# Kernel optimization log

Hardware: AMD Instinct MI355X
Metric: run time of the kernel (lower is better)

Reference implementation:

```python
import jax, jax.numpy as jnp
import numpy as np

N, D, E, NNZ = 200000, 128, 1024, 1600000


def setup_inputs() -> dict:
    key = jax.random.key(0)
    ks = jax.random.split(key, 8)
    x = jax.random.normal(ks[0], (N, D), jnp.float32)
    tb_W = jax.random.normal(ks[1], (5, 3, D, D), jnp.float32) * 0.05
    tb_b = jax.random.normal(ks[2], (5, 3, D), jnp.float32) * 0.05
    hg_W = jax.random.normal(ks[3], (2, D, D), jnp.float32) * 0.05
    hg_b = jax.random.normal(ks[4], (2, D), jnp.float32) * 0.05
    hyperedge_attr = jax.random.normal(ks[5], (E, D), jnp.float32)
    node_idx = jax.random.randint(ks[6], (NNZ,), 0, N)
    edge_idx = jax.random.randint(ks[7], (NNZ,), 0, E)
    return dict(x=x, tb_W=tb_W, tb_b=tb_b, hg_W=hg_W, hg_b=hg_b,
                hyperedge_attr=hyperedge_attr, node_idx=node_idx,
                edge_idx=edge_idx, num_hyperedges=E)


def _time_block(x, W, b):
    # 1x1 Conv2d over channel dim == per-node linear. W:[3,D,D], b:[3,D]
    c1 = x @ W[0] + b[0]
    c2 = x @ W[1] + b[1]
    c3 = x @ W[2] + b[2]
    return jax.nn.relu(c1 + jax.nn.sigmoid(c2) + c3)


def _hypergraph_conv(x, node_idx, edge_idx, W, b, num_nodes, num_edges):
    # PyG HypergraphConv, use_attention=False (heads=1):
    # out = D^{-1} H B H^T (x W) + b, H given as COO (node_idx, edge_idx)
    xp = x @ W
    ones = jnp.ones(node_idx.shape[0], xp.dtype)
    Dn = jax.ops.segment_sum(ones, node_idx, num_segments=num_nodes)
    Dn = jnp.where(Dn > 0, 1.0 / Dn, 0.0)
    Be = jax.ops.segment_sum(ones, edge_idx, num_segments=num_edges)
    Be = jnp.where(Be > 0, 1.0 / Be, 0.0)
    # node -> hyperedge aggregation, normalized by 1/B_e
    m = jax.ops.segment_sum(xp[node_idx], edge_idx, num_segments=num_edges) * Be[:, None]
    # hyperedge -> node aggregation, normalized by 1/D_v
    out = jax.ops.segment_sum(m[edge_idx], node_idx, num_segments=num_nodes) * Dn[:, None]
    return out + b


def reference(x, tb_W, tb_b, hg_W, hg_b, hyperedge_attr, node_idx, edge_idx, num_hyperedges):
    # hyperedge_attr is unused when use_attention=False (faithful to PyG)
    n = x.shape[0]
    h = _time_block(x, tb_W[0], tb_b[0])
    h = _hypergraph_conv(h, node_idx, edge_idx, hg_W[0], hg_b[0], n, num_hyperedges)
    h = _time_block(h, tb_W[1], tb_b[1])
    h = _time_block(h, tb_W[2], tb_b[2])
    h = _hypergraph_conv(h, node_idx, edge_idx, hg_W[1], hg_b[1], n, num_hyperedges)
    h = _time_block(h, tb_W[3], tb_b[3])
    h = _time_block(h, tb_W[4], tb_b[4])
    return h
```

## Files before the change

kernel.cpp:

```cpp
#include <hip/hip_runtime.h>
#include <stdint.h>

#define N_NODES 200000
#define DIM     128
#define N_EDGES 1024
#define NNZ_C   1600000
#define NT_TILES 6250

#define NBLK   250
#define CHUNK  6400
#define ITERS  25
#define NCB    196

#define NG_BLOCKS 2048
#define NG_WAVES  (NG_BLOCKS*4)

typedef __attribute__((ext_vector_type(8))) short short8;
typedef __attribute__((ext_vector_type(4))) float f32x4;

__device__ __forceinline__ float u2f(uint32_t u){ union{uint32_t u;float f;} x; x.u=u; return x.f; }
__device__ __forceinline__ uint32_t f2u(float f){ union{uint32_t u;float f;} x; x.f=f; return x.u; }
__device__ __forceinline__ unsigned short f2bf(float f){
  uint32_t u = f2u(f);
  u += 0x7fffu + ((u >> 16) & 1u);
  return (unsigned short)(u >> 16);
}

__global__ void prep_tb_w(const float* __restrict__ W, short* __restrict__ Wt){
  int i = blockIdx.x*256 + threadIdx.x;
  if (i >= 5*384*128) return;
  int k   = i & 127;
  int col = (i >> 7) % 384;
  int s   = i / 49152;
  int j = col >> 7, n = col & 127;
  Wt[i] = (short)f2bf(W[((s*3 + j)*128 + k)*128 + n]);
}
__global__ void prep_hg_wf(const float* __restrict__ W, float* __restrict__ Wtf){
  int i = blockIdx.x*256 + threadIdx.x;
  if (i >= 2*128*128) return;
  int k = i & 127;
  int n = (i >> 7) & 127;
  int g = i >> 14;
  Wtf[i] = W[(g*128 + k)*128 + n];
}

__global__ __launch_bounds__(256) void hist_kernel(
    const int* __restrict__ nidx, const int* __restrict__ eidx,
    int* __restrict__ ebh, int* __restrict__ nbh)
{
  __shared__ int eh[N_EDGES];
  __shared__ int nh[NCB];
  int tid = threadIdx.x, blk = blockIdx.x;
  #pragma unroll
  for (int l = tid; l < N_EDGES; l += 256) eh[l] = 0;
  for (int l = tid; l < NCB; l += 256) nh[l] = 0;
  __syncthreads();
  int base = blk*CHUNK;
  for (int it = 0; it < ITERS; it++){
    int i = base + it*256 + tid;
    atomicAdd(&eh[eidx[i]], 1);
    atomicAdd(&nh[nidx[i] >> 10], 1);
  }
  __syncthreads();
  for (int l = tid; l < N_EDGES; l += 256) ebh[blk*N_EDGES + l] = eh[l];
  for (int l = tid; l < NCB; l += 256) nbh[blk*NCB + l] = nh[l];
}

__global__ __launch_bounds__(1024) void escan_kernel(
    int* __restrict__ ebh, int* __restrict__ eoff)
{
  __shared__ int sc[1024];
  int e = threadIdx.x;
  int total = 0;
  #pragma unroll 10
  for (int b = 0; b < NBLK; b++){
    int idx = b*N_EDGES + e;
    int t = ebh[idx];
    ebh[idx] = total;
    total += t;
  }
  sc[e] = total; __syncthreads();
  for (int off=1; off<1024; off<<=1){
    int v = (e >= off) ? sc[e-off] : 0;
    __syncthreads();
    sc[e] += v;
    __syncthreads();
  }
  int base = sc[e] - total;
  eoff[e] = base;
  if (e == 1023) eoff[1024] = sc[1023];
  #pragma unroll 10
  for (int b = 0; b < NBLK; b++) ebh[b*N_EDGES + e] += base;
}

__global__ __launch_bounds__(256) void nscan_kernel(
    int* __restrict__ nbh, int* __restrict__ cbase)
{
  __shared__ int sc[256];
  int c = threadIdx.x;
  int total = 0;
  if (c < NCB){
    #pragma unroll 10
    for (int b = 0; b < NBLK; b++){
      int idx = b*NCB + c;
      int t = nbh[idx];
      nbh[idx] = total;
      total += t;
    }
  }
  sc[c] = (c < NCB) ? total : 0; __syncthreads();
  for (int off=1; off<256; off<<=1){
    int v = (c >= off) ? sc[c-off] : 0;
    __syncthreads();
    sc[c] += v;
    __syncthreads();
  }
  int base = sc[c] - ((c < NCB) ? total : 0);
  if (c < NCB) cbase[c] = base;
  if (c == NCB-1) cbase[NCB] = sc[c];
  __syncthreads();
  if (c < NCB){
    #pragma unroll 10
    for (int b = 0; b < NBLK; b++) nbh[b*NCB + c] += base;
  }
}

__global__ __launch_bounds__(256) void scatter_kernel(
    const int* __restrict__ nidx, const int* __restrict__ eidx,
    const int* __restrict__ ebh, const int* __restrict__ nbh,
    int* __restrict__ enodes, uint32_t* __restrict__ pairs)
{
  __shared__ int cure[N_EDGES];
  __shared__ int curn[NCB];
  int tid = threadIdx.x, blk = blockIdx.x;
  for (int l = tid; l < N_EDGES; l += 256) cure[l] = ebh[blk*N_EDGES + l];
  for (int l = tid; l < NCB; l += 256)     curn[l] = nbh[blk*NCB + l];
  __syncthreads();
  int base = blk*CHUNK;
  for (int it = 0; it < ITERS; it++){
    int i = base + it*256 + tid;
    int v = nidx[i], e = eidx[i];
    int pe = atomicAdd(&cure[e], 1);
    enodes[pe] = v;
    int pn = atomicAdd(&curn[v >> 10], 1);
    pairs[pn] = ((uint32_t)v << 10) | (uint32_t)e;
  }
}

__global__ __launch_bounds__(256) void node_build_kernel(
    const uint32_t* __restrict__ pairs, const int* __restrict__ cbase,
    int* __restrict__ noff, int* __restrict__ nedges)
{
  __shared__ int cnt[1024];
  __shared__ int off[1024];
  __shared__ int part[256];
  int tid = threadIdx.x, c = blockIdx.x;
  int n0 = c << 10;
  int nloc = min(1024, N_NODES - n0);
  int s = cbase[c], e = cbase[c+1];
  #pragma unroll
  for (int l = tid; l < 1024; l += 256) cnt[l] = 0;
  __syncthreads();
  for (int i = s + tid; i < e; i += 256)
    atomicAdd(&cnt[(pairs[i] >> 10) & 1023], 1);
  __syncthreads();
  int c0 = cnt[tid*4], c1 = cnt[tid*4+1], c2 = cnt[tid*4+2], c3 = cnt[tid*4+3];
  int sum = c0+c1+c2+c3;
  part[tid] = sum; __syncthreads();
  for (int o=1; o<256; o<<=1){
    int v = (tid >= o) ? part[tid-o] : 0;
    __syncthreads();
    part[tid] += v;
    __syncthreads();
  }
  int pb = part[tid] - sum;
  off[tid*4]   = pb;
  off[tid*4+1] = pb + c0;
  off[tid*4+2] = pb + c0 + c1;
  off[tid*4+3] = pb + c0 + c1 + c2;
  __syncthreads();
  for (int l = tid; l < nloc; l += 256) noff[n0 + l] = s + off[l];
  if (c == 0 && tid == 0) noff[N_NODES] = NNZ_C;
  __syncthreads();
  for (int i = s + tid; i < e; i += 256){
    uint32_t p = pairs[i];
    int local = (p >> 10) & 1023;
    int pos = s + atomicAdd(&off[local], 1);
    nedges[pos] = (int)(p & 1023);
  }
}

template<bool IN_F32, int OUT_MODE>
__global__ __launch_bounds__(256, 2) void gemm_kernel(
    const void* __restrict__ in, void* __restrict__ out,
    const short* __restrict__ Wt, const float* __restrict__ bias)
{
  __shared__ short Atile[32][136];
  const int tid  = threadIdx.x;
  const int lane = tid & 63;
  const int w    = tid >> 6;
  const int l15  = lane & 15;
  const int quad = lane >> 4;

  short8 bfrag[3][2][4];
  #pragma unroll
  for (int j = 0; j < 3; j++)
    #pragma unroll
    for (int nt = 0; nt < 2; nt++){
      const short* bp = Wt + (j*128 + w*32 + nt*16 + l15)*128 + quad*8;
      #pragma unroll
      for (int ks = 0; ks < 4; ks++)
        bfrag[j][nt][ks] = *(const short8*)(bp + ks*32);
    }

  float bv[3][2];
  #pragma unroll
  for (int j = 0; j < 3; j++)
    #pragma unroll
    for (int nt = 0; nt < 2; nt++)
      bv[j][nt] = bias[j*128 + w*32 + nt*16 + l15];

  const int arow = tid >> 3;
  const int aseg = (tid & 7) * 2;

  short8 pre0, pre1;
  auto loadA = [&](int t){
    int off = (t*32 + arow)*128 + aseg*8;
    if (IN_F32){
      const float* f = (const float*)in + off;
      f32x4 q0 = ((const f32x4*)f)[0];
      f32x4 q1 = ((const f32x4*)f)[1];
      f32x4 q2 = ((const f32x4*)f)[2];
      f32x4 q3 = ((const f32x4*)f)[3];
      short8 t0, t1;
      #pragma unroll
      for (int u = 0; u < 4; u++){
        t0[u]   = (short)f2bf(q0[u]);
        t0[u+4] = (short)f2bf(q1[u]);
        t1[u]   = (short)f2bf(q2[u]);
        t1[u+4] = (short)f2bf(q3[u]);
      }
      pre0 = t0; pre1 = t1;
    } else {
      const short* hp = (const short*)in + off;
      pre0 = *(const short8*)hp;
      pre1 = *(const short8*)(hp + 8);
    }
  };

  int t = blockIdx.x;
  loadA(t);
  for (;;){
    __syncthreads();
    *(short8*)&Atile[arow][aseg*8]     = pre0;
    *(short8*)&Atile[arow][aseg*8 + 8] = pre1;
    __syncthreads();
    int tn = t + gridDim.x;
    if (tn < NT_TILES) loadA(tn);

    const int base = t*32;
    #pragma unroll
    for (int rt = 0; rt < 2; rt++){
      short8 af[4];
      #pragma unroll
      for (int ks = 0; ks < 4; ks++)
        af[ks] = *(const short8*)&Atile[rt*16 + l15][ks*32 + quad*8];

      f32x4 acc[3][2];
      #pragma unroll
      for (int j = 0; j < 3; j++)
        #pragma unroll
        for (int nt = 0; nt < 2; nt++){
          acc[j][nt] = (f32x4){0.f, 0.f, 0.f, 0.f};
          #pragma unroll
          for (int ks = 0; ks < 4; ks++)
            acc[j][nt] = __builtin_amdgcn_mfma_f32_16x16x32_bf16(
                af[ks], bfrag[j][nt][ks], acc[j][nt], 0, 0, 0);
        }

      #pragma unroll
      for (int nt = 0; nt < 2; nt++){
        int col = w*32 + nt*16 + l15;
        #pragma unroll
        for (int r = 0; r < 4; r++){
          int row = base + rt*16 + quad*4 + r;
          float c2 = acc[1][nt][r] + bv[1][nt];
          float sg = 1.f / (1.f + __expf(-c2));
          float v = acc[0][nt][r] + bv[0][nt] + sg + acc[2][nt][r] + bv[2][nt];
          v = fmaxf(v, 0.f);
          if (OUT_MODE == 1) ((float*)out)[row*128 + col] = v;
          else if (OUT_MODE == 0) ((unsigned short*)out)[row*128 + col] = f2bf(v);
          else {
            int pk = __builtin_amdgcn_cvt_pk_fp8_f32(v, v, 0, false);
            ((unsigned char*)out)[row*128 + col] = (unsigned char)(pk & 0xff);
          }
        }
      }
    }
    if (tn >= NT_TILES) break;
    t = tn;
  }
}

__global__ __launch_bounds__(256) void edge_gather_kernel(
    const unsigned char* __restrict__ h8, const int* __restrict__ eoff,
    const int* __restrict__ enodes, float* __restrict__ s_e)
{
  int bid = blockIdx.x;
  int e = bid >> 2, q = bid & 3;
  int s = eoff[e], en = eoff[e+1];
  int tid = threadIdx.x;
  int rr   = tid >> 5;
  int slot = q*8 + rr;
  int ch   = tid & 31;
  float a0=0.f, a1=0.f, a2=0.f, a3=0.f;
  int i = s + slot;
  int nd = (i < en) ? enodes[i] : 0;
  while (i < en){
    int inx = i + 32;
    int ndn = (inx < en) ? enodes[inx] : 0;
    uint32_t raw = *(const uint32_t*)(h8 + (size_t)nd*128 + ch*4);
    auto lo = __builtin_amdgcn_cvt_pk_f32_fp8(raw, false);
    auto hi = __builtin_amdgcn_cvt_pk_f32_fp8(raw, true);
    a0 += lo[0]; a1 += lo[1]; a2 += hi[0]; a3 += hi[1];
    i = inx; nd = ndn;
  }
  __shared__ float red[8][132];
  red[rr][ch*4+0]=a0; red[rr][ch*4+1]=a1; red[rr][ch*4+2]=a2; red[rr][ch*4+3]=a3;
  __syncthreads();
  if (tid < 128){
    float sum = 0.f;
    #pragma unroll
    for (int r = 0; r < 8; r++) sum += red[r][tid];
    atomicAdd(&s_e[e*128 + tid], sum);
  }
}

__global__ __launch_bounds__(128) void egemm_kernel(
    const float* __restrict__ s_e, const int* __restrict__ eoff,
    const float* __restrict__ Wtf, uint32_t* __restrict__ mbf)
{
  __shared__ float srow[128];
  __shared__ float sacc[128];
  int e = blockIdx.x, n = threadIdx.x;
  srow[n] = s_e[e*128 + n];
  __syncthreads();
  int deg = eoff[e+1] - eoff[e];
  float be = deg > 0 ? 1.f/(float)deg : 0.f;
  const f32x4* w4 = (const f32x4*)(Wtf + n*128);
  float acc = 0.f;
  #pragma unroll
  for (int k = 0; k < 32; k++){
    f32x4 qv = w4[k];
    acc += qv[0]*srow[k*4] + qv[1]*srow[k*4+1] + qv[2]*srow[k*4+2] + qv[3]*srow[k*4+3];
  }
  sacc[n] = acc * be;
  __syncthreads();
  if (n < 64){
    uint32_t lo = f2bf(sacc[2*n]);
    uint32_t hi = f2bf(sacc[2*n+1]);
    mbf[e*64 + n] = (hi << 16) | lo;
  }
}

__global__ __launch_bounds__(256) void node_gather_kernel(
    const uint32_t* __restrict__ mbf, const int* __restrict__ noff,
    const int* __restrict__ nedges, const float* __restrict__ hb,
    uint32_t* __restrict__ outp)
{
  int wid  = (blockIdx.x << 2) | (threadIdx.x >> 6);
  int lane = threadIdx.x & 63;
  float b0 = hb[2*lane], b1 = hb[2*lane+1];
  const int K = (N_NODES + NG_WAVES - 1) / NG_WAVES;
  int v0 = wid * K;
  int v1 = min(v0 + K, N_NODES);
  for (int v = v0; v < v1; v++){
    int s = noff[v], e = noff[v+1];
    float a0 = 0.f, a1 = 0.f, a2 = 0.f, a3 = 0.f;
    int i = s;
    for (; i + 4 <= e; i += 4){
      int e0 = nedges[i],   e1 = nedges[i+1];
      int e2 = nedges[i+2], e3 = nedges[i+3];
      uint32_t r0 = mbf[(e0 << 6) | lane];
      uint32_t r1 = mbf[(e1 << 6) | lane];
      uint32_t r2 = mbf[(e2 << 6) | lane];
      uint32_t r3 = mbf[(e3 << 6) | lane];
      a0 += u2f(r0 << 16); a1 += u2f(r0 & 0xffff0000u);
      a2 += u2f(r1 << 16); a3 += u2f(r1 & 0xffff0000u);
      a0 += u2f(r2 << 16); a1 += u2f(r2 & 0xffff0000u);
      a2 += u2f(r3 << 16); a3 += u2f(r3 & 0xffff0000u);
    }
    for (; i < e; i++){
      int ed = nedges[i];
      uint32_t r = mbf[(ed << 6) | lane];
      a0 += u2f(r << 16); a1 += u2f(r & 0xffff0000u);
    }
    a0 += a2; a1 += a3;
    float dn = (e > s) ? 1.f/(float)(e - s) : 0.f;
    uint32_t lo = f2bf(a0*dn + b0);
    uint32_t hi = f2bf(a1*dn + b1);
    outp[((size_t)v << 6) | lane] = (hi << 16) | lo;
  }
}

extern "C" void kernel_launch(void* const* d_in, const int* in_sizes, int n_in,
                              void* d_out, int out_size, void* d_ws, size_t ws_size,
                              hipStream_t stream)
{
  (void)in_sizes; (void)n_in; (void)out_size; (void)ws_size;
  const float* x   = (const float*)d_in[0];
  const float* tbW = (const float*)d_in[1];
  const float* tbb = (const float*)d_in[2];
  const float* hgW = (const float*)d_in[3];
  const float* hgb = (const float*)d_in[4];
  const int* nidx  = (const int*)d_in[6];
  const int* eidx  = (const int*)d_in[7];
  float* out = (float*)d_out;

  char* p = (char*)d_ws;
  auto alloc = [&](size_t sz){ void* r = (void*)p; p += (sz + 255) & ~(size_t)255; return r; };
  unsigned short* hA = (unsigned short*)alloc((size_t)N_NODES*DIM*2);
  unsigned short* hB = (unsigned short*)alloc((size_t)N_NODES*DIM*2);
  unsigned char*  h8 = (unsigned char*)alloc((size_t)N_NODES*DIM);
  float* s_e  = (float*)alloc((size_t)N_EDGES*DIM*4);
  uint32_t* mbf = (uint32_t*)alloc((size_t)N_EDGES*64*4);
  short* WtTb = (short*)alloc((size_t)5*384*128*2);
  float* Wtf  = (float*)alloc((size_t)2*128*128*4);
  int* ebh  = (int*)alloc((size_t)NBLK*N_EDGES*4);
  int* nbh  = (int*)alloc((size_t)NBLK*NCB*4);
  int* eoff = (int*)alloc((N_EDGES+1)*4);
  int* cbase= (int*)alloc((NCB+1)*4);
  int* noff = (int*)alloc((size_t)(N_NODES+1)*4);
  int* enodes = (int*)alloc((size_t)NNZ_C*4);
  int* nedges = (int*)alloc((size_t)NNZ_C*4);
  uint32_t* pairs = (uint32_t*)h8;

  prep_tb_w<<<960, 256, 0, stream>>>(tbW, WtTb);
  prep_hg_wf<<<128, 256, 0, stream>>>(hgW, Wtf);

  hist_kernel<<<NBLK, 256, 0, stream>>>(nidx, eidx, ebh, nbh);
  escan_kernel<<<1, 1024, 0, stream>>>(ebh, eoff);
  nscan_kernel<<<1, 256, 0, stream>>>(nbh, cbase);
  scatter_kernel<<<NBLK, 256, 0, stream>>>(nidx, eidx, ebh, nbh, enodes, pairs);
  node_build_kernel<<<NCB, 256, 0, stream>>>(pairs, cbase, noff, nedges);

  gemm_kernel<true, 2><<<1024, 256, 0, stream>>>(x, h8, WtTb, tbb);
  hipMemsetAsync(s_e, 0, (size_t)N_EDGES*DIM*4, stream);
  edge_gather_kernel<<<4*N_EDGES, 256, 0, stream>>>(h8, eoff, enodes, s_e);
  egemm_kernel<<<N_EDGES, 128, 0, stream>>>(s_e, eoff, Wtf, mbf);
  node_gather_kernel<<<NG_BLOCKS, 256, 0, stream>>>(mbf, noff, nedges, hgb, (uint32_t*)hA);
  gemm_kernel<false, 0><<<1024, 256, 0, stream>>>(hA, hB, WtTb + 1*49152, tbb + 1*384);
  gemm_kernel<false, 2><<<1024, 256, 0, stream>>>(hB, h8, WtTb + 2*49152, tbb + 2*384);
  hipMemsetAsync(s_e, 0, (size_t)N_EDGES*DIM*4, stream);
  edge_gather_kernel<<<4*N_EDGES, 256, 0, stream>>>(h8, eoff, enodes, s_e);
  egemm_kernel<<<N_EDGES, 128, 0, stream>>>(s_e, eoff, Wtf + 16384, mbf);
  node_gather_kernel<<<NG_BLOCKS, 256, 0, stream>>>(mbf, noff, nedges, hgb + 128, (uint32_t*)hA);
  gemm_kernel<false, 0><<<1024, 256, 0, stream>>>(hA, hB, WtTb + 3*49152, tbb + 3*384);
  gemm_kernel<false, 1><<<1024, 256, 0, stream>>>(hB, out, WtTb + 4*49152, tbb + 4*384);
}
```

Before: 768.1 us.

## Restructure edge gather: one block per edge, 16-byte loads, no atomics

```diff
diff --git a/kernel.cpp b/kernel.cpp
--- a/kernel.cpp
+++ b/kernel.cpp
@@ -302,37 +302,68 @@
   }
 }
 
+__device__ __forceinline__ void acc16(float* a, uint4 r){
+  uint32_t w[4] = {r.x, r.y, r.z, r.w};
+  #pragma unroll
+  for (int q = 0; q < 4; q++){
+    auto lo = __builtin_amdgcn_cvt_pk_f32_fp8(w[q], false);
+    auto hi = __builtin_amdgcn_cvt_pk_f32_fp8(w[q], true);
+    a[q*4+0] += lo[0]; a[q*4+1] += lo[1]; a[q*4+2] += hi[0]; a[q*4+3] += hi[1];
+  }
+}
+
 __global__ __launch_bounds__(256) void edge_gather_kernel(
     const unsigned char* __restrict__ h8, const int* __restrict__ eoff,
     const int* __restrict__ enodes, float* __restrict__ s_e)
 {
-  int bid = blockIdx.x;
-  int e = bid >> 2, q = bid & 3;
+  int e = blockIdx.x;
   int s = eoff[e], en = eoff[e+1];
-  int tid = threadIdx.x;
-  int rr   = tid >> 5;
-  int slot = q*8 + rr;
-  int ch   = tid & 31;
-  float a0=0.f, a1=0.f, a2=0.f, a3=0.f;
-  int i = s + slot;
-  int nd = (i < en) ? enodes[i] : 0;
-  while (i < en){
-    int inx = i + 32;
-    int ndn = (inx < en) ? enodes[inx] : 0;
-    uint32_t raw = *(const uint32_t*)(h8 + (size_t)nd*128 + ch*4);
-    auto lo = __builtin_amdgcn_cvt_pk_f32_fp8(raw, false);
-    auto hi = __builtin_amdgcn_cvt_pk_f32_fp8(raw, true);
-    a0 += lo[0]; a1 += lo[1]; a2 += hi[0]; a3 += hi[1];
-    i = inx; nd = ndn;
-  }
-  __shared__ float red[8][132];
-  red[rr][ch*4+0]=a0; red[rr][ch*4+1]=a1; red[rr][ch*4+2]=a2; red[rr][ch*4+3]=a3;
+  int tid  = threadIdx.x;
+  int slot = tid >> 3;
+  int ch   = tid & 7;
+  const size_t choff = (size_t)ch * 16;
+
+  float a[16];
+  #pragma unroll
+  for (int j = 0; j < 16; j++) a[j] = 0.f;
+
+  int i0 = s + slot;
+  int n0 = (i0      < en) ? enodes[i0]      : -1;
+  int n1 = (i0 + 32 < en) ? enodes[i0 + 32] : -1;
+  int n2 = (i0 + 64 < en) ? enodes[i0 + 64] : -1;
+  int n3 = (i0 + 96 < en) ? enodes[i0 + 96] : -1;
+
+  while (i0 < en){
+    int i1 = i0 + 128;
+    int m0 = (i1      < en) ? enodes[i1]      : -1;
+    int m1 = (i1 + 32 < en) ? enodes[i1 + 32] : -1;
+    int m2 = (i1 + 64 < en) ? enodes[i1 + 64] : -1;
+    int m3 = (i1 + 96 < en) ? enodes[i1 + 96] : -1;
+
+    uint4 r0 = *(const uint4*)(h8 + (((size_t)max(n0,0)) << 7) + choff);
+    uint4 r1 = *(const uint4*)(h8 + (((size_t)max(n1,0)) << 7) + choff);
+    uint4 r2 = *(const uint4*)(h8 + (((size_t)max(n2,0)) << 7) + choff);
+    uint4 r3 = *(const uint4*)(h8 + (((size_t)max(n3,0)) << 7) + choff);
+    if (n0 < 0) r0 = make_uint4(0,0,0,0);
+    if (n1 < 0) r1 = make_uint4(0,0,0,0);
+    if (n2 < 0) r2 = make_uint4(0,0,0,0);
+    if (n3 < 0) r3 = make_uint4(0,0,0,0);
+
+    acc16(a, r0); acc16(a, r1); acc16(a, r2); acc16(a, r3);
+
+    n0 = m0; n1 = m1; n2 = m2; n3 = m3;
+    i0 = i1;
+  }
+
+  __shared__ float red[32][132];
+  #pragma unroll
+  for (int j = 0; j < 16; j++) red[slot][ch*16 + j] = a[j];
   __syncthreads();
   if (tid < 128){
     float sum = 0.f;
     #pragma unroll
-    for (int r = 0; r < 8; r++) sum += red[r][tid];
-    atomicAdd(&s_e[e*128 + tid], sum);
+    for (int r = 0; r < 32; r++) sum += red[r][tid];
+    s_e[e*128 + tid] = sum;
   }
 }
 
@@ -445,14 +476,12 @@
   node_build_kernel<<<NCB, 256, 0, stream>>>(pairs, cbase, noff, nedges);
 
   gemm_kernel<true, 2><<<1024, 256, 0, stream>>>(x, h8, WtTb, tbb);
-  hipMemsetAsync(s_e, 0, (size_t)N_EDGES*DIM*4, stream);
-  edge_gather_kernel<<<4*N_EDGES, 256, 0, stream>>>(h8, eoff, enodes, s_e);
+  edge_gather_kernel<<<N_EDGES, 256, 0, stream>>>(h8, eoff, enodes, s_e);
   egemm_kernel<<<N_EDGES, 128, 0, stream>>>(s_e, eoff, Wtf, mbf);
   node_gather_kernel<<<NG_BLOCKS, 256, 0, stream>>>(mbf, noff, nedges, hgb, (uint32_t*)hA);
   gemm_kernel<false, 0><<<1024, 256, 0, stream>>>(hA, hB, WtTb + 1*49152, tbb + 1*384);
   gemm_kernel<false, 2><<<1024, 256, 0, stream>>>(hB, h8, WtTb + 2*49152, tbb + 2*384);
-  hipMemsetAsync(s_e, 0, (size_t)N_EDGES*DIM*4, stream);
-  edge_gather_kernel<<<4*N_EDGES, 256, 0, stream>>>(h8, eoff, enodes, s_e);
+  edge_gather_kernel<<<N_EDGES, 256, 0, stream>>>(h8, eoff, enodes, s_e);
   egemm_kernel<<<N_EDGES, 128, 0, stream>>>(s_e, eoff, Wtf + 16384, mbf);
   node_gather_kernel<<<NG_BLOCKS, 256, 0, stream>>>(mbf, noff, nedges, hgb + 128, (uint32_t*)hA);
   gemm_kernel<false, 0><<<1024, 256, 0, stream>>>(hA, hB, WtTb + 3*49152, tbb + 3*384);
```

Measured after the change: 681.4 us. 11.3% less time.
